# Kernel optimization log

Hardware: AMD Instinct MI355X
Metric: run time of the kernel (lower is better)

## Reference

```python
import jax, jax.numpy as jnp
import numpy as np

N = 50000
D = 256
E = 800000


def setup_inputs() -> dict:
    key = jax.random.key(0)
    ks = jax.random.split(key, 9)
    X = jax.random.normal(ks[0], (N, D), dtype=jnp.float32)
    edge_index = jax.random.randint(ks[1], (2, E), 0, N, dtype=jnp.int32)
    edge_weight = jax.random.uniform(ks[2], (E,), dtype=jnp.float32)
    p = jax.random.normal(ks[3], (D,), dtype=jnp.float32)
    s = 1.0 / np.sqrt(D)
    W_ih = jax.random.normal(ks[4], (3 * D, D), dtype=jnp.float32) * s
    W_hh = jax.random.normal(ks[5], (3 * D, D), dtype=jnp.float32) * s
    b_ih = jax.random.normal(ks[6], (3 * D,), dtype=jnp.float32) * s
    b_hh = jax.random.normal(ks[7], (3 * D,), dtype=jnp.float32) * s
    W0 = jax.random.normal(ks[8], (D, D), dtype=jnp.float32) * s
    return {"X": X, "edge_index": edge_index, "edge_weight": edge_weight,
            "p": p, "W_ih": W_ih, "W_hh": W_hh, "b_ih": b_ih, "b_hh": b_hh, "W0": W0}


def reference(X, edge_index, edge_weight, p, W_ih, W_hh, b_ih, b_hh, W0):
    n, d = X.shape  # n=N, d=D; ratio = d/n -> TopK keeps k=d nodes
    k = d

    # ---- TopKPooling: score = X.p/||p||, keep top-k, gate by tanh(score) ----
    score = X @ p / jnp.linalg.norm(p)          # [n]
    top_score, idx = jax.lax.top_k(score, k)    # [k]
    x_tilde = X[idx] * jnp.tanh(top_score)[:, None]  # [k, d]

    # ---- Single-step GRU: input x_tilde (batch=k=d), hidden = conv weight W0 [d,d] ----
    h = W0
    gi = x_tilde @ W_ih.T + b_ih                # [d, 3d]
    gh = h @ W_hh.T + b_hh                      # [d, 3d]
    i_r, i_z, i_n = jnp.split(gi, 3, axis=1)
    h_r, h_z, h_n = jnp.split(gh, 3, axis=1)
    r = jax.nn.sigmoid(i_r + h_r)
    z = jax.nn.sigmoid(i_z + h_z)
    nn_ = jnp.tanh(i_n + r * h_n)
    W_new = (1.0 - z) * nn_ + z * h             # evolved conv weight [d, d]

    # ---- GCNConv (no bias): x = X @ W, symmetric norm with self-loops ----
    xw = X @ W_new                              # [n, d]
    src, dst = edge_index[0], edge_index[1]
    loop = jnp.arange(n, dtype=src.dtype)
    src_f = jnp.concatenate([src, loop])
    dst_f = jnp.concatenate([dst, loop])
    ew_f = jnp.concatenate([edge_weight, jnp.ones((n,), dtype=X.dtype)])
    deg = jax.ops.segment_sum(ew_f, dst_f, num_segments=n)  # [n]
    dinv = jnp.where(deg > 0, jax.lax.rsqrt(deg), 0.0)
    norm = dinv[src_f] * ew_f * dinv[dst_f]     # [E+n]
    msgs = norm[:, None] * xw[src_f]            # [E+n, d] gather
    out = jax.ops.segment_sum(msgs, dst_f, num_segments=n)  # scatter-add
    return out
```

## Files before the change

kernel.cpp:

```cpp
#include <hip/hip_runtime.h>
#include <cstdint>
#include <cstddef>

#define N_NODES 50000
#define DIM     256
#define NEDGE   800000
#define TOPK    256
#define HBINS   65536
#define CAND_CAP 2048
#define SLOT    64
#define SROWS   32

typedef unsigned long long u64;
typedef float f32x4 __attribute__((ext_vector_type(4)));
typedef __bf16 b16x8 __attribute__((ext_vector_type(8)));
typedef unsigned short us8 __attribute__((ext_vector_type(8)));

__device__ __forceinline__ u64 okey(double d) {
  u64 b = (u64)__double_as_longlong(d);
  return (b & 0x8000000000000000ULL) ? ~b : (b | 0x8000000000000000ULL);
}

__device__ __forceinline__ unsigned short f2bf(float f) {
  unsigned u = __float_as_uint(f);
  return (unsigned short)((u + 0x7fffu + ((u >> 16) & 1u)) >> 16);
}

__device__ __forceinline__ float bf2f(unsigned short u) {
  return __uint_as_float(((unsigned)u) << 16);
}

__global__ __launch_bounds__(256) void init_kernel(unsigned* __restrict__ w, int nwords) {
  int stride = gridDim.x * 256;
  for (int i = blockIdx.x * 256 + threadIdx.x; i < nwords; i += stride) w[i] = 0u;
}

__global__ __launch_bounds__(256) void score_kernel(const float* __restrict__ X,
                             const float* __restrict__ p,
                             double* __restrict__ scores, unsigned* __restrict__ hist) {
  __shared__ double part[SROWS][65];
  int tid = threadIdx.x;
  int lane = tid & 63, wid = tid >> 6;
  float4 p4 = reinterpret_cast<const float4*>(p)[lane];
  int nblk_rows = gridDim.x * SROWS;
  for (int rb = blockIdx.x * SROWS; rb < N_NODES; rb += nblk_rows) {
    int r0 = rb + wid * 8;
    float4 x[8];
#pragma unroll
    for (int u = 0; u < 8; ++u) {
      int r = r0 + u;
      x[u] = (r < N_NODES)
           ? reinterpret_cast<const float4*>(X + (size_t)r * DIM)[lane]
           : make_float4(0.f, 0.f, 0.f, 0.f);
    }
#pragma unroll
    for (int u = 0; u < 8; ++u) {
      double s = (double)x[u].x * p4.x + (double)x[u].y * p4.y +
                 (double)x[u].z * p4.z + (double)x[u].w * p4.w;
      part[wid * 8 + u][lane] = s;
    }
    __syncthreads();
    if (tid < SROWS) {
      int row = rb + tid;
      if (row < N_NODES) {
        const double* pr = part[tid];
        double a0 = 0.0, a1 = 0.0, a2 = 0.0, a3 = 0.0;
#pragma unroll
        for (int l = 0; l < 64; l += 4) {
          a0 += pr[l + 0]; a1 += pr[l + 1]; a2 += pr[l + 2]; a3 += pr[l + 3];
        }
        double s = (a0 + a1) + (a2 + a3);
        scores[row] = s;
        unsigned bin = (unsigned)(okey(s) >> 48);
        atomicAdd(&hist[bin], 1u);
      }
    }
    __syncthreads();
  }
}

__global__ __launch_bounds__(1024) void findbin_kernel(const unsigned* __restrict__ hist,
                                                       int* __restrict__ ctrl) {
  __shared__ int sums[1024];
  int t = threadIdx.x;
  int base = t * 64;
  const uint4* h4 = reinterpret_cast<const uint4*>(hist + base);
  int s = 0;
#pragma unroll
  for (int i = 0; i < 16; ++i) {
    uint4 v = h4[i];
    s += (int)(v.x + v.y + v.z + v.w);
  }
  sums[t] = s;
  __syncthreads();
  for (int off = 1; off < 1024; off <<= 1) {
    int x = (t + off < 1024) ? sums[t + off] : 0;
    __syncthreads();
    sums[t] += x;
    __syncthreads();
  }
  int S_incl = sums[t];
  int S_excl = S_incl - s;
  if (S_excl < TOPK && S_incl >= TOPK) {
    int c = S_excl;
    int thr = base;
    for (int b = base + 63; b >= base; --b) {
      c += (int)hist[b];
      if (c >= TOPK) { thr = b; break; }
    }
    ctrl[0] = thr;
  }
}

__global__ void collect_kernel(const double* __restrict__ scores, int* __restrict__ ctrl,
                               double* __restrict__ cand_s, int* __restrict__ cand_i) {
  int i = blockIdx.x * 256 + threadIdx.x;
  if (i >= N_NODES) return;
  double sc = scores[i];
  int bin = (int)(okey(sc) >> 48);
  if (bin >= ctrl[0]) {
    int pos = atomicAdd(&ctrl[1], 1);
    if (pos < CAND_CAP) { cand_s[pos] = sc; cand_i[pos] = i; }
  }
}

__global__ __launch_bounds__(1024) void sort_kernel(const int* __restrict__ ctrl,
                                                    const double* __restrict__ cand_s,
                                                    const int* __restrict__ cand_i,
                                                    const float* __restrict__ p,
                                                    int* __restrict__ top_idx,
                                                    float* __restrict__ gate) {
  __shared__ double cs[CAND_CAP];
  __shared__ int ci[CAND_CAP];
  __shared__ double pred[256];
  int t = threadIdx.x;
  if (t < 256) {
    double v = (double)p[t];
    pred[t] = v * v;
  }
  int cnt = ctrl[1];
  if (cnt > CAND_CAP) cnt = CAND_CAP;
  int M = (cnt <= 1024) ? 1024 : CAND_CAP;
  for (int s = 0; s < M / 1024; ++s) {
    int i = t + s * 1024;
    if (i < cnt) { cs[i] = cand_s[i]; ci[i] = cand_i[i]; }
    else         { cs[i] = -1e308;    ci[i] = 0x7fffffff; }
  }
  __syncthreads();
  if (t < 128) pred[t] += pred[t + 128];
  __syncthreads();
  if (t < 64) pred[t] += pred[t + 64];
  __syncthreads();
  if (t < 32) { pred[t] += pred[t + 32]; }
  __syncthreads();
  if (t == 0) {
    double acc = 0.0;
    for (int i = 0; i < 32; ++i) acc += pred[i];
    pred[0] = sqrt(acc);
  }
  for (int k2 = 2; k2 <= M; k2 <<= 1) {
    for (int j = k2 >> 1; j > 0; j >>= 1) {
      for (int s = 0; s < M / 1024; ++s) {
        int i = t + s * 1024;
        int ixj = i ^ j;
        if (ixj > i) {
          double si = cs[i], sx = cs[ixj];
          int ii = ci[i], ix = ci[ixj];
          bool up = ((i & k2) == 0);
          bool sw = up ? ((sx > si) || (sx == si && ix < ii))
                       : ((si > sx) || (si == sx && ii < ix));
          if (sw) { cs[i] = sx; cs[ixj] = si; ci[i] = ix; ci[ixj] = ii; }
        }
      }
      __syncthreads();
    }
  }
  if (t < TOPK) {
    top_idx[t] = ci[t];
    gate[t] = (float)tanh(cs[t] / pred[0]);
  }
}

__global__ __launch_bounds__(256) void gru_gemm_kernel(const float* __restrict__ X,
                                const int* __restrict__ top_idx, const float* __restrict__ gate,
                                const float* __restrict__ W0,
                                const float* __restrict__ W_ih, const float* __restrict__ W_hh,
                                const float* __restrict__ b_ih, const float* __restrict__ b_hh,
                                float* __restrict__ gi, float* __restrict__ gh) {
  __shared__ float As[8][DIM];
  int tid = threadIdx.x;
  int c = blockIdx.x * 256 + tid;
  int r0 = blockIdx.y * 8;
  int which = blockIdx.z;
  const float* W = which ? W_hh : W_ih;
  const float* b = which ? b_hh : b_ih;
  float* outp = which ? gh : gi;
  if (which) {
    const float4* src = reinterpret_cast<const float4*>(W0 + (size_t)r0 * DIM);
    float4* dst = reinterpret_cast<float4*>(&As[0][0]);
    dst[tid] = src[tid];
    dst[tid + 256] = src[tid + 256];
  } else {
#pragma unroll
    for (int h = 0; h < 2; ++h) {
      int idx2 = tid + h * 256;
      int r = idx2 >> 6;
      int e = idx2 & 63;
      int srcrow = top_idx[r0 + r];
      float g = gate[r0 + r];
      float4 v = reinterpret_cast<const float4*>(X + (size_t)srcrow * DIM)[e];
      v.x *= g; v.y *= g; v.z *= g; v.w *= g;
      reinterpret_cast<float4*>(&As[0][0])[idx2] = v;
    }
  }
  __syncthreads();
  const float4* Wr = reinterpret_cast<const float4*>(W + (size_t)c * DIM);
  float acc[8] = {0, 0, 0, 0, 0, 0, 0, 0};
#pragma unroll 4
  for (int k4 = 0; k4 < DIM / 4; ++k4) {
    float4 w = Wr[k4];
#pragma unroll
    for (int r = 0; r < 8; ++r) {
      acc[r] += As[r][k4 * 4 + 0] * w.x + As[r][k4 * 4 + 1] * w.y +
                As[r][k4 * 4 + 2] * w.z + As[r][k4 * 4 + 3] * w.w;
    }
  }
  float bc = b[c];
#pragma unroll
  for (int r = 0; r < 8; ++r)
    outp[(size_t)(r0 + r) * 768 + c] = acc[r] + bc;
}

__global__ void wnew_kernel(const float* __restrict__ gi, const float* __restrict__ gh,
                            const float* __restrict__ W0, unsigned short* __restrict__ Wnbt) {
  int rr = blockIdx.x, c = threadIdx.x;
  const float* gir = gi + (size_t)rr * 768;
  const float* ghr = gh + (size_t)rr * 768;
  float i_r = gir[c],       h_r = ghr[c];
  float i_z = gir[c + 256], h_z = ghr[c + 256];
  float i_n = gir[c + 512], h_n = ghr[c + 512];
  float r = 1.f / (1.f + expf(-(i_r + h_r)));
  float z = 1.f / (1.f + expf(-(i_z + h_z)));
  float nn = tanhf(i_n + r * h_n);
  float h = W0[(size_t)rr * DIM + c];
  float w = (1.f - z) * nn + z * h;
  Wnbt[(size_t)c * DIM + rr] = f2bf(w);
}

__global__ __launch_bounds__(256) void xw_mfma_kernel(const float* __restrict__ X,
                                                      const unsigned short* __restrict__ Wnbt,
                                                      unsigned short* __restrict__ xwb) {
  int wid = threadIdx.x >> 6, lane = threadIdx.x & 63;
  int r0 = blockIdx.x * 64 + wid * 16;
  if (r0 >= N_NODES) return;
  int rowA = r0 + (lane & 15);
  int kgrp = lane >> 4;
  int koff = kgrp * 8;

  const float4* Ar = reinterpret_cast<const float4*>(X + (size_t)rowA * DIM);
  b16x8 afr[8];
#pragma unroll
  for (int kt = 0; kt < 8; ++kt) {
    float4 f0 = Ar[kt * 8 + kgrp * 2 + 0];
    float4 f1 = Ar[kt * 8 + kgrp * 2 + 1];
    union { us8 u; b16x8 b; } cv;
    cv.u[0] = f2bf(f0.x); cv.u[1] = f2bf(f0.y); cv.u[2] = f2bf(f0.z); cv.u[3] = f2bf(f0.w);
    cv.u[4] = f2bf(f1.x); cv.u[5] = f2bf(f1.y); cv.u[6] = f2bf(f1.z); cv.u[7] = f2bf(f1.w);
    afr[kt] = cv.b;
  }

  int colB = lane & 15;
  const unsigned short* Bbase = Wnbt + (size_t)colB * DIM + koff;
  int rr = r0 + kgrp * 4;
#pragma unroll 4
  for (int nf = 0; nf < 16; ++nf) {
    f32x4 acc = {0.f, 0.f, 0.f, 0.f};
    const unsigned short* Bp = Bbase + (size_t)nf * 16 * DIM;
#pragma unroll
    for (int kt = 0; kt < 8; ++kt) {
      b16x8 bfr = *reinterpret_cast<const b16x8*>(Bp + kt * 32);
      acc = __builtin_amdgcn_mfma_f32_16x16x32_bf16(afr[kt], bfr, acc, 0, 0, 0);
    }
    int cc = nf * 16 + colB;
#pragma unroll
    for (int j = 0; j < 4; ++j)
      xwb[(size_t)(rr + j) * DIM + cc] = f2bf(acc[j]);
  }
}

__global__ __launch_bounds__(256) void scatter_kernel(const int* __restrict__ ei,
                               const float* __restrict__ ew,
                               float* __restrict__ deg,
                               int* __restrict__ fill, u64* __restrict__ colval) {
  int stride = gridDim.x * 256;
  for (int e = blockIdx.x * 256 + threadIdx.x; e < NEDGE; e += stride) {
    int s = ei[e], d = ei[NEDGE + e];
    float w = ew[e];
    atomicAdd(&deg[d], w);
    int pos = atomicAdd(&fill[d], 1);
    if (pos < SLOT)
      colval[(size_t)d * SLOT + pos] = ((u64)__float_as_uint(w) << 32) | (unsigned)s;
  }
}

__global__ __launch_bounds__(256) void agg_kernel(const unsigned short* __restrict__ xwb,
                           const float* __restrict__ deg,
                           const int* __restrict__ fill, const u64* __restrict__ colval,
                           float* __restrict__ out) {
  int lane = threadIdx.x & 63;
  int gw = blockIdx.x * 4 + (threadIdx.x >> 6);
  int nw = gridDim.x * 4;
  for (int i = gw; i < N_NODES; i += nw) {
    float di = __frsqrt_rn(deg[i] + 1.0f);
    ushort4 sv = reinterpret_cast<const ushort4*>(xwb + (size_t)i * DIM)[lane];
    float4 acc;
    acc.x = di * bf2f(sv.x); acc.y = di * bf2f(sv.y);
    acc.z = di * bf2f(sv.z); acc.w = di * bf2f(sv.w);
    int n = fill[i];
    if (n > SLOT) n = SLOT;
    const u64* cv = colval + (size_t)i * SLOT;
    int j = 0;
    for (; j + 8 <= n; j += 8) {
      u64 a[8];
#pragma unroll
      for (int u = 0; u < 8; ++u) a[u] = cv[j + u];
      unsigned c[8];
      ushort4 m[8];
      float dg[8];
#pragma unroll
      for (int u = 0; u < 8; ++u) {
        c[u] = (unsigned)a[u];
        m[u] = reinterpret_cast<const ushort4*>(xwb + (size_t)c[u] * DIM)[lane];
        dg[u] = deg[c[u]];
      }
#pragma unroll
      for (int u = 0; u < 8; ++u) {
        float v = __uint_as_float((unsigned)(a[u] >> 32)) * __frsqrt_rn(dg[u] + 1.0f);
        acc.x += v * bf2f(m[u].x); acc.y += v * bf2f(m[u].y);
        acc.z += v * bf2f(m[u].z); acc.w += v * bf2f(m[u].w);
      }
    }
    for (; j < n; ++j) {
      u64 a0 = cv[j];
      unsigned c0 = (unsigned)a0;
      ushort4 m0 = reinterpret_cast<const ushort4*>(xwb + (size_t)c0 * DIM)[lane];
      float v0 = __uint_as_float((unsigned)(a0 >> 32)) * __frsqrt_rn(deg[c0] + 1.0f);
      acc.x += v0 * bf2f(m0.x); acc.y += v0 * bf2f(m0.y);
      acc.z += v0 * bf2f(m0.z); acc.w += v0 * bf2f(m0.w);
    }
    acc.x *= di; acc.y *= di; acc.z *= di; acc.w *= di;
    reinterpret_cast<float4*>(out + (size_t)i * DIM)[lane] = acc;
  }
}

extern "C" void kernel_launch(void* const* d_in, const int* in_sizes, int n_in,
                              void* d_out, int out_size, void* d_ws, size_t ws_size,
                              hipStream_t stream) {
  const float* X    = (const float*)d_in[0];
  const int*   ei   = (const int*)d_in[1];
  const float* ew   = (const float*)d_in[2];
  const float* p    = (const float*)d_in[3];
  const float* W_ih = (const float*)d_in[4];
  const float* W_hh = (const float*)d_in[5];
  const float* b_ih = (const float*)d_in[6];
  const float* b_hh = (const float*)d_in[7];
  const float* W0   = (const float*)d_in[8];
  float* out = (float*)d_out;

  char* ws = (char*)d_ws;
  size_t off = 0;
  auto alloc = [&](size_t bytes) { size_t o = off; off = (off + bytes + 255) & ~(size_t)255; return o; };

  size_t hist_o  = alloc(HBINS * 4);
  size_t ctrl_o  = alloc(64);
  size_t deg_o   = alloc(N_NODES * 4);
  size_t fill_o  = alloc(N_NODES * 4);
  size_t zero_span = off;
  size_t scores_o = alloc(N_NODES * 8);
  size_t cands_o  = alloc(CAND_CAP * 8);
  size_t candi_o  = alloc(CAND_CAP * 4);
  size_t topidx_o = alloc(TOPK * 4);
  size_t gate_o   = alloc(TOPK * 4);
  size_t gi_o     = alloc((size_t)256 * 768 * 4);
  size_t gh_o     = alloc((size_t)256 * 768 * 4);
  size_t wnbt_o   = alloc((size_t)DIM * DIM * 2);
  size_t colval_o = alloc((size_t)N_NODES * SLOT * 8);
  size_t xwb_o    = alloc((size_t)N_NODES * DIM * 2);
  (void)ws_size; (void)n_in; (void)in_sizes; (void)out_size;

  unsigned* hist  = (unsigned*)(ws + hist_o);
  int*    ctrl    = (int*)(ws + ctrl_o);
  float*  deg     = (float*)(ws + deg_o);
  int*    fill    = (int*)(ws + fill_o);
  double* scores  = (double*)(ws + scores_o);
  double* cand_s  = (double*)(ws + cands_o);
  int*    cand_i  = (int*)(ws + candi_o);
  int*    top_idx = (int*)(ws + topidx_o);
  float*  gate    = (float*)(ws + gate_o);
  float*  gi      = (float*)(ws + gi_o);
  float*  gh      = (float*)(ws + gh_o);
  unsigned short* Wnbt = (unsigned short*)(ws + wnbt_o);
  u64*    colval  = (u64*)(ws + colval_o);
  unsigned short* xwb = (unsigned short*)(ws + xwb_o);

  init_kernel<<<256, 256, 0, stream>>>((unsigned*)ws, (int)(zero_span / 4));
  score_kernel<<<391, 256, 0, stream>>>(X, p, scores, hist);
  findbin_kernel<<<1, 1024, 0, stream>>>(hist, ctrl);
  collect_kernel<<<(N_NODES + 255) / 256, 256, 0, stream>>>(scores, ctrl, cand_s, cand_i);
  sort_kernel<<<1, 1024, 0, stream>>>(ctrl, cand_s, cand_i, p, top_idx, gate);
  gru_gemm_kernel<<<dim3(3, 32, 2), 256, 0, stream>>>(X, top_idx, gate, W0, W_ih, W_hh,
                                                      b_ih, b_hh, gi, gh);
  wnew_kernel<<<256, 256, 0, stream>>>(gi, gh, W0, Wnbt);
  xw_mfma_kernel<<<(N_NODES + 63) / 64, 256, 0, stream>>>(X, Wnbt, xwb);
  scatter_kernel<<<1024, 256, 0, stream>>>(ei, ew, deg, fill, colval);
  agg_kernel<<<2048, 256, 0, stream>>>(xwb, deg, fill, colval, out);
}
```

Baseline: 434.1 us.

## Widen score rows per block, batch scatter atomics, nontemporal agg stores

The score kernel now handles 64 rows per block with 16 rows per wave and reduces each row with four threads plus shuffles instead of 32 serial threads, launched on half as many blocks. The scatter kernel unrolls eight edges per thread so loads and atomics are issued in batches, on fewer blocks. The aggregation output is written with nontemporal stores to avoid polluting cache. These target latency and serialization in the small pre-processing kernels, at the cost of higher register use and fewer blocks.

Result: slower. 466.6 us (+7.5%).

```diff
diff --git a/kernel.cpp b/kernel.cpp
--- a/kernel.cpp
+++ b/kernel.cpp
@@ -9,7 +9,7 @@
 #define HBINS   65536
 #define CAND_CAP 2048
 #define SLOT    64
-#define SROWS   32
+#define SROWS   64
 
 typedef unsigned long long u64;
 typedef float f32x4 __attribute__((ext_vector_type(4)));
@@ -44,35 +44,37 @@
   float4 p4 = reinterpret_cast<const float4*>(p)[lane];
   int nblk_rows = gridDim.x * SROWS;
   for (int rb = blockIdx.x * SROWS; rb < N_NODES; rb += nblk_rows) {
-    int r0 = rb + wid * 8;
-    float4 x[8];
-#pragma unroll
-    for (int u = 0; u < 8; ++u) {
+    int r0 = rb + wid * 16;
+    float4 x[16];
+#pragma unroll
+    for (int u = 0; u < 16; ++u) {
       int r = r0 + u;
       x[u] = (r < N_NODES)
            ? reinterpret_cast<const float4*>(X + (size_t)r * DIM)[lane]
            : make_float4(0.f, 0.f, 0.f, 0.f);
     }
 #pragma unroll
-    for (int u = 0; u < 8; ++u) {
+    for (int u = 0; u < 16; ++u) {
       double s = (double)x[u].x * p4.x + (double)x[u].y * p4.y +
                  (double)x[u].z * p4.z + (double)x[u].w * p4.w;
-      part[wid * 8 + u][lane] = s;
+      part[wid * 16 + u][lane] = s;
     }
     __syncthreads();
-    if (tid < SROWS) {
-      int row = rb + tid;
-      if (row < N_NODES) {
-        const double* pr = part[tid];
-        double a0 = 0.0, a1 = 0.0, a2 = 0.0, a3 = 0.0;
-#pragma unroll
-        for (int l = 0; l < 64; l += 4) {
-          a0 += pr[l + 0]; a1 += pr[l + 1]; a2 += pr[l + 2]; a3 += pr[l + 3];
-        }
-        double s = (a0 + a1) + (a2 + a3);
-        scores[row] = s;
-        unsigned bin = (unsigned)(okey(s) >> 48);
-        atomicAdd(&hist[bin], 1u);
+    {
+      int lr = tid >> 2, seg = tid & 3;
+      int row = rb + lr;
+      const double* pr = part[lr] + seg * 16;
+      double a0 = 0.0, a1 = 0.0, a2 = 0.0, a3 = 0.0;
+#pragma unroll
+      for (int l = 0; l < 16; l += 4) {
+        a0 += pr[l + 0]; a1 += pr[l + 1]; a2 += pr[l + 2]; a3 += pr[l + 3];
+      }
+      double a = (a0 + a1) + (a2 + a3);
+      a += __shfl_xor(a, 1, 64);
+      a += __shfl_xor(a, 2, 64);
+      if (seg == 0 && row < N_NODES) {
+        scores[row] = a;
+        atomicAdd(&hist[(unsigned)(okey(a) >> 48)], 1u);
       }
     }
     __syncthreads();
@@ -293,7 +295,30 @@
                                float* __restrict__ deg,
                                int* __restrict__ fill, u64* __restrict__ colval) {
   int stride = gridDim.x * 256;
-  for (int e = blockIdx.x * 256 + threadIdx.x; e < NEDGE; e += stride) {
+  int e = blockIdx.x * 256 + threadIdx.x;
+  for (; e + 7 * stride < NEDGE; e += 8 * stride) {
+    int s[8], d[8];
+    float w[8];
+#pragma unroll
+    for (int u = 0; u < 8; ++u) {
+      s[u] = ei[e + u * stride];
+      d[u] = ei[NEDGE + e + u * stride];
+      w[u] = ew[e + u * stride];
+    }
+    int pos[8];
+#pragma unroll
+    for (int u = 0; u < 8; ++u) {
+      atomicAdd(&deg[d[u]], w[u]);
+      pos[u] = atomicAdd(&fill[d[u]], 1);
+    }
+#pragma unroll
+    for (int u = 0; u < 8; ++u) {
+      if (pos[u] < SLOT)
+        colval[(size_t)d[u] * SLOT + pos[u]] =
+            ((u64)__float_as_uint(w[u]) << 32) | (unsigned)s[u];
+    }
+  }
+  for (; e < NEDGE; e += stride) {
     int s = ei[e], d = ei[NEDGE + e];
     float w = ew[e];
     atomicAdd(&deg[d], w);
@@ -313,7 +338,7 @@
   for (int i = gw; i < N_NODES; i += nw) {
     float di = __frsqrt_rn(deg[i] + 1.0f);
     ushort4 sv = reinterpret_cast<const ushort4*>(xwb + (size_t)i * DIM)[lane];
-    float4 acc;
+    f32x4 acc;
     acc.x = di * bf2f(sv.x); acc.y = di * bf2f(sv.y);
     acc.z = di * bf2f(sv.z); acc.w = di * bf2f(sv.w);
     int n = fill[i];
@@ -349,7 +374,7 @@
       acc.z += v0 * bf2f(m0.z); acc.w += v0 * bf2f(m0.w);
     }
     acc.x *= di; acc.y *= di; acc.z *= di; acc.w *= di;
-    reinterpret_cast<float4*>(out + (size_t)i * DIM)[lane] = acc;
+    __builtin_nontemporal_store(acc, reinterpret_cast<f32x4*>(out + (size_t)i * DIM) + lane);
   }
 }
 
@@ -404,7 +429,7 @@
   unsigned short* xwb = (unsigned short*)(ws + xwb_o);
 
   init_kernel<<<256, 256, 0, stream>>>((unsigned*)ws, (int)(zero_span / 4));
-  score_kernel<<<391, 256, 0, stream>>>(X, p, scores, hist);
+  score_kernel<<<196, 256, 0, stream>>>(X, p, scores, hist);
   findbin_kernel<<<1, 1024, 0, stream>>>(hist, ctrl);
   collect_kernel<<<(N_NODES + 255) / 256, 256, 0, stream>>>(scores, ctrl, cand_s, cand_i);
   sort_kernel<<<1, 1024, 0, stream>>>(ctrl, cand_s, cand_i, p, top_idx, gate);
@@ -412,6 +437,6 @@
                                                       b_ih, b_hh, gi, gh);
   wnew_kernel<<<256, 256, 0, stream>>>(gi, gh, W0, Wnbt);
   xw_mfma_kernel<<<(N_NODES + 63) / 64, 256, 0, stream>>>(X, Wnbt, xwb);
-  scatter_kernel<<<1024, 256, 0, stream>>>(ei, ew, deg, fill, colval);
+  scatter_kernel<<<384, 256, 0, stream>>>(ei, ew, deg, fill, colval);
   agg_kernel<<<2048, 256, 0, stream>>>(xwb, deg, fill, colval, out);
 }
```
